# Performance work log

Hardware: AMD Instinct MI355X
Metric: run time of the kernel (lower is better)

The kernel has to match this reference:

```python
import jax, jax.numpy as jnp
import numpy as np

N, D = 8192, 256
TEMP = 0.07


def setup_inputs() -> dict:
    key = jax.random.key(0)
    kx, ky = jax.random.split(key)
    x = jax.random.normal(kx, (N, D), dtype=jnp.float32)
    y = jax.random.normal(ky, (N, D), dtype=jnp.float32)
    # L2-normalize (standard for InfoNCE; keeps exp(sim/temp) finite)
    x = x / jnp.linalg.norm(x, axis=-1, keepdims=True)
    y = y / jnp.linalg.norm(y, axis=-1, keepdims=True)
    return {"x": x, "y": y}


def reference(x, y):
    # sim_matrix = exp(x @ y^T / temperature), shape [N, N]
    sim = jnp.exp(jnp.matmul(x, y.T) / TEMP)
    # positives: exp(<x_i, y_i>/T) == diagonal of sim
    l_pos = jnp.exp(jnp.sum(x * y, axis=-1) / TEMP)
    # negatives: row-sum excluding the diagonal (equivalent to masked_select)
    l_neg = jnp.sum(sim, axis=-1) - jnp.diagonal(sim)
    loss = jnp.mean(-jnp.log(l_pos / l_neg))
    return loss
```

## Files before the change

kernel.cpp:

```cpp
#include <hip/hip_runtime.h>
#include <hip/hip_bf16.h>

#define N_ROWS 8192
#define D_DIM  256

static constexpr float kQuantScale = 64.0f;
static constexpr float kScaleAcc = 20.609929155556627f / 4096.0f;
static constexpr float kInvTAcc  = 14.285714285714286f / 4096.0f;

typedef float f32x4 __attribute__((ext_vector_type(4)));
typedef int   i32x4 __attribute__((ext_vector_type(4)));
typedef int   i32x8 __attribute__((ext_vector_type(8)));

__device__ __forceinline__ void gl_lds16(const void* g, void* l) {
  __builtin_amdgcn_global_load_lds(
      (const __attribute__((address_space(1))) void*)g,
      (__attribute__((address_space(3))) void*)l, 16, 0, 0);
}

__global__ __launch_bounds__(256)
void cvt_fp8_kernel(const float* __restrict__ x, const float* __restrict__ y,
                    unsigned char* __restrict__ xq, unsigned char* __restrict__ yq,
                    float* __restrict__ rowsum, unsigned int* __restrict__ done) {
  if (blockIdx.x == 0) {
    for (int i = threadIdx.x; i < N_ROWS; i += 256) rowsum[i] = 0.f;
    if (threadIdx.x == 0) *done = 0u;
  }
  const int per_mat = N_ROWS * D_DIM / 8;
  int idx = blockIdx.x * blockDim.x + threadIdx.x;
  const float* src = x;
  unsigned char* dst = xq;
  int i = idx;
  if (idx >= per_mat) { src = y; dst = yq; i = idx - per_mat; }
  float4 a = ((const float4*)src)[2 * (size_t)i];
  float4 b = ((const float4*)src)[2 * (size_t)i + 1];
  int v0 = 0, v1 = 0;
  v0 = __builtin_amdgcn_cvt_pk_fp8_f32(a.x * kQuantScale, a.y * kQuantScale, v0, false);
  v0 = __builtin_amdgcn_cvt_pk_fp8_f32(a.z * kQuantScale, a.w * kQuantScale, v0, true);
  v1 = __builtin_amdgcn_cvt_pk_fp8_f32(b.x * kQuantScale, b.y * kQuantScale, v1, false);
  v1 = __builtin_amdgcn_cvt_pk_fp8_f32(b.z * kQuantScale, b.w * kQuantScale, v1, true);
  *(int2*)(dst + (size_t)i * 8) = make_int2(v0, v1);
}

__global__ __launch_bounds__(512, 1)
void infonce_gemm(const unsigned char* __restrict__ X,
                  const unsigned char* __restrict__ Y,
                  float* __restrict__ rowsum, float* __restrict__ diag,
                  unsigned int* __restrict__ done, float* __restrict__ out) {
  __shared__ unsigned char Xs[256 * 256];
  __shared__ unsigned char Ys[2][128 * 256];
  __shared__ unsigned int ticket_s;

  const int b  = blockIdx.x;
  const int bi = b >> 3;
  const int gj = b & 7;

  const int t    = threadIdx.x;
  const int lane = t & 63;
  const int wave = t >> 6;
  const int wm   = wave >> 1;
  const int wn   = wave & 1;
  const int quad = lane >> 4;
  const int l15  = lane & 15;

  const unsigned char* Xblk = X + (size_t)(bi * 256) * D_DIM;

#pragma unroll
  for (int it = 0; it < 8; ++it) {
    const int c0  = (it * 8 + wave) * 64;
    const int s   = c0 + lane;
    const int row = s >> 4;
    const int cg  = (s & 15) ^ (row & 15);
    gl_lds16(Xblk + (size_t)row * D_DIM + cg * 16, &Xs[c0 * 16]);
  }
  {
    const unsigned char* Yblk = Y + (size_t)(gj * 8) * 128 * D_DIM;
#pragma unroll
    for (int it = 0; it < 4; ++it) {
      const int c0  = (it * 8 + wave) * 64;
      const int s   = c0 + lane;
      const int row = s >> 4;
      const int cg  = (s & 15) ^ (row & 15);
      gl_lds16(Yblk + (size_t)row * D_DIM + cg * 16, &Ys[0][c0 * 16]);
    }
  }

  f32x4 acc[4][4];
#pragma unroll
  for (int a = 0; a < 4; ++a)
#pragma unroll
    for (int c = 0; c < 4; ++c) acc[a][c] = (f32x4){0.f, 0.f, 0.f, 0.f};

  float psum[4][4];
#pragma unroll
  for (int a = 0; a < 4; ++a)
#pragma unroll
    for (int c = 0; c < 4; ++c) psum[a][c] = 0.f;

  for (int tt = 0; tt < 8; ++tt) {
    const int p = tt & 1;

    __syncthreads();

    if (tt < 7) {
      const unsigned char* Yblk = Y + (size_t)(gj * 8 + tt + 1) * 128 * D_DIM;
#pragma unroll
      for (int it = 0; it < 4; ++it) {
        const int c0  = (it * 8 + wave) * 64;
        const int s   = c0 + lane;
        const int row = s >> 4;
        const int cg  = (s & 15) ^ (row & 15);
        gl_lds16(Yblk + (size_t)row * D_DIM + cg * 16, &Ys[p ^ 1][c0 * 16]);
      }
    }

#pragma unroll
    for (int kb = 0; kb < 2; ++kb) {
      i32x8 a8[4], b8[4];
#pragma unroll
      for (int mt = 0; mt < 4; ++mt) {
        const int row = wm * 64 + mt * 16 + l15;
        const int p0  = (kb * 8 + quad * 2 + 0) ^ (row & 15);
        const int p1  = (kb * 8 + quad * 2 + 1) ^ (row & 15);
        i32x4 lo = *(const i32x4*)(&Xs[row * 256 + p0 * 16]);
        i32x4 hi = *(const i32x4*)(&Xs[row * 256 + p1 * 16]);
        a8[mt] = __builtin_shufflevector(lo, hi, 0, 1, 2, 3, 4, 5, 6, 7);
      }
#pragma unroll
      for (int nt = 0; nt < 4; ++nt) {
        const int row = wn * 64 + nt * 16 + l15;
        const int p0  = (kb * 8 + quad * 2 + 0) ^ (row & 15);
        const int p1  = (kb * 8 + quad * 2 + 1) ^ (row & 15);
        i32x4 lo = *(const i32x4*)(&Ys[p][row * 256 + p0 * 16]);
        i32x4 hi = *(const i32x4*)(&Ys[p][row * 256 + p1 * 16]);
        b8[nt] = __builtin_shufflevector(lo, hi, 0, 1, 2, 3, 4, 5, 6, 7);
      }
#pragma unroll
      for (int mt = 0; mt < 4; ++mt)
#pragma unroll
        for (int nt = 0; nt < 4; ++nt)
          acc[mt][nt] = __builtin_amdgcn_mfma_scale_f32_16x16x128_f8f6f4(
              a8[mt], b8[nt], acc[mt][nt],
              0, 0,
              0, 0x7F7F7F7F,
              0, 0x7F7F7F7F);
    }

#pragma unroll
    for (int mt = 0; mt < 4; ++mt) {
#pragma unroll
      for (int rr = 0; rr < 4; ++rr) {
        float part = 0.f;
#pragma unroll
        for (int nt = 0; nt < 4; ++nt)
          part += __builtin_amdgcn_exp2f(acc[mt][nt][rr] * kScaleAcc);
        psum[mt][rr] += part;
      }
    }
    {
      const int ct = gj * 8 + tt;
      const bool d0 = (ct == 2 * bi)     && (wm == wn);
      const bool d1 = (ct == 2 * bi + 1) && (wm == wn + 2);
      if (d0 || d1) {
        const int gi_base = bi * 256 + wm * 64;
#pragma unroll
        for (int nt = 0; nt < 4; ++nt)
#pragma unroll
          for (int rr = 0; rr < 4; ++rr)
            if (l15 == quad * 4 + rr)
              atomicExch(&diag[gi_base + nt * 16 + l15], acc[nt][nt][rr]);
      }
    }
#pragma unroll
    for (int a = 0; a < 4; ++a)
#pragma unroll
      for (int c = 0; c < 4; ++c) acc[a][c] = (f32x4){0.f, 0.f, 0.f, 0.f};
  }

  {
    const int gi_base = bi * 256 + wm * 64;
#pragma unroll
    for (int mt = 0; mt < 4; ++mt) {
#pragma unroll
      for (int rr = 0; rr < 4; ++rr) {
        float v = psum[mt][rr];
        v += __shfl_xor(v, 1);
        v += __shfl_xor(v, 2);
        v += __shfl_xor(v, 4);
        v += __shfl_xor(v, 8);
        if (l15 == 0)
          atomicAdd(&rowsum[gi_base + mt * 16 + quad * 4 + rr], v);
      }
    }
  }

  __syncthreads();
  if (t == 0) ticket_s = atomicAdd(done, 1u);
  __syncthreads();
  if (ticket_s == 255u) {
    __threadfence();
    float local = 0.f;
    for (int i = t; i < N_ROWS; i += 512) {
      const float rs = atomicAdd(&rowsum[i], 0.0f);
      const float d  = atomicAdd(&diag[i], 0.0f);
      local += __logf(rs - __builtin_amdgcn_exp2f(d * kScaleAcc)) - d * kInvTAcc;
    }
    float* red = (float*)Xs;
    red[t] = local;
    __syncthreads();
    for (int s2 = 256; s2 > 0; s2 >>= 1) {
      if (t < s2) red[t] += red[t + s2];
      __syncthreads();
    }
    if (t == 0) out[0] = red[0] / (float)N_ROWS;
  }
}

extern "C" void kernel_launch(void* const* d_in, const int* in_sizes, int n_in,
                              void* d_out, int out_size, void* d_ws, size_t ws_size,
                              hipStream_t stream) {
  const float* x = (const float*)d_in[0];
  const float* y = (const float*)d_in[1];
  float* out = (float*)d_out;

  float* rowsum = (float*)d_ws;
  float* diag   = rowsum + N_ROWS;
  unsigned int* done = (unsigned int*)(diag + N_ROWS);
  unsigned char* xq = (unsigned char*)d_ws + 2 * N_ROWS * sizeof(float) + 16;
  unsigned char* yq = xq + (size_t)N_ROWS * D_DIM;

  int cvt_blocks = 2 * N_ROWS * D_DIM / 8 / 256;
  cvt_fp8_kernel<<<cvt_blocks, 256, 0, stream>>>(x, y, xq, yq, rowsum, done);

  infonce_gemm<<<256, 512, 0, stream>>>(xq, yq, rowsum, diag, done, out);
}
```

Before: 101.0 us.

## Add dedicated producer wave for LDS loads with flag-based sync

Adds a ninth wave that performs all global-to-LDS copies of the X and Y tiles, signaling compute waves via LDS ready/consumed counters instead of __syncthreads. Compute waves spin on flags and never issue loads, aiming to overlap loading with MFMA work and remove barrier stalls. The single producer wave serializes loads that previously were spread across eight waves, which may lengthen the prologue; spin-waiting adds scheduling overhead.

```diff
diff --git a/kernel.cpp b/kernel.cpp
--- a/kernel.cpp
+++ b/kernel.cpp
@@ -42,13 +42,15 @@
   *(int2*)(dst + (size_t)i * 8) = make_int2(v0, v1);
 }
 
-__global__ __launch_bounds__(512, 1)
+__global__ __launch_bounds__(576, 1)
 void infonce_gemm(const unsigned char* __restrict__ X,
                   const unsigned char* __restrict__ Y,
                   float* __restrict__ rowsum, float* __restrict__ diag,
                   unsigned int* __restrict__ done, float* __restrict__ out) {
   __shared__ unsigned char Xs[256 * 256];
   __shared__ unsigned char Ys[2][128 * 256];
+  __shared__ int ready[2];
+  __shared__ int consumed[2];
   __shared__ unsigned int ticket_s;
 
   const int b  = blockIdx.x;
@@ -63,133 +65,146 @@
   const int quad = lane >> 4;
   const int l15  = lane & 15;
 
-  const unsigned char* Xblk = X + (size_t)(bi * 256) * D_DIM;
-
-#pragma unroll
-  for (int it = 0; it < 8; ++it) {
-    const int c0  = (it * 8 + wave) * 64;
-    const int s   = c0 + lane;
-    const int row = s >> 4;
-    const int cg  = (s & 15) ^ (row & 15);
-    gl_lds16(Xblk + (size_t)row * D_DIM + cg * 16, &Xs[c0 * 16]);
-  }
-  {
-    const unsigned char* Yblk = Y + (size_t)(gj * 8) * 128 * D_DIM;
-#pragma unroll
-    for (int it = 0; it < 4; ++it) {
-      const int c0  = (it * 8 + wave) * 64;
+  if (t == 0) { ready[0] = -1; ready[1] = -1; consumed[0] = 0; consumed[1] = 0; }
+  __syncthreads();
+
+  if (wave == 8) {
+    const unsigned char* Xblk = X + (size_t)(bi * 256) * D_DIM;
+    for (int it = 0; it < 64; ++it) {
+      const int c0  = it * 64;
       const int s   = c0 + lane;
       const int row = s >> 4;
       const int cg  = (s & 15) ^ (row & 15);
-      gl_lds16(Yblk + (size_t)row * D_DIM + cg * 16, &Ys[0][c0 * 16]);
-    }
-  }
-
-  f32x4 acc[4][4];
-#pragma unroll
-  for (int a = 0; a < 4; ++a)
-#pragma unroll
-    for (int c = 0; c < 4; ++c) acc[a][c] = (f32x4){0.f, 0.f, 0.f, 0.f};
-
-  float psum[4][4];
-#pragma unroll
-  for (int a = 0; a < 4; ++a)
-#pragma unroll
-    for (int c = 0; c < 4; ++c) psum[a][c] = 0.f;
-
-  for (int tt = 0; tt < 8; ++tt) {
-    const int p = tt & 1;
-
-    __syncthreads();
-
-    if (tt < 7) {
-      const unsigned char* Yblk = Y + (size_t)(gj * 8 + tt + 1) * 128 * D_DIM;
-#pragma unroll
-      for (int it = 0; it < 4; ++it) {
-        const int c0  = (it * 8 + wave) * 64;
+      gl_lds16(Xblk + (size_t)row * D_DIM + cg * 16, &Xs[c0 * 16]);
+    }
+    {
+      const unsigned char* Yblk = Y + (size_t)(gj * 8) * 128 * D_DIM;
+      for (int it = 0; it < 32; ++it) {
+        const int c0  = it * 64;
         const int s   = c0 + lane;
         const int row = s >> 4;
         const int cg  = (s & 15) ^ (row & 15);
-        gl_lds16(Yblk + (size_t)row * D_DIM + cg * 16, &Ys[p ^ 1][c0 * 16]);
-      }
-    }
-
-#pragma unroll
-    for (int kb = 0; kb < 2; ++kb) {
-      i32x8 a8[4], b8[4];
+        gl_lds16(Yblk + (size_t)row * D_DIM + cg * 16, &Ys[0][c0 * 16]);
+      }
+    }
+    __builtin_amdgcn_s_waitcnt(0);
+    __hip_atomic_store(&ready[0], 0, __ATOMIC_RELEASE, __HIP_MEMORY_SCOPE_WORKGROUP);
+    for (int r = 1; r < 8; ++r) {
+      const int bb = r & 1;
+      if (r >= 2) {
+        const int need = 8 * (r >> 1);
+        while (__hip_atomic_load(&consumed[bb], __ATOMIC_ACQUIRE,
+                                 __HIP_MEMORY_SCOPE_WORKGROUP) < need)
+          __builtin_amdgcn_s_sleep(2);
+      }
+      const unsigned char* Yblk = Y + (size_t)(gj * 8 + r) * 128 * D_DIM;
+      for (int it = 0; it < 32; ++it) {
+        const int c0  = it * 64;
+        const int s   = c0 + lane;
+        const int row = s >> 4;
+        const int cg  = (s & 15) ^ (row & 15);
+        gl_lds16(Yblk + (size_t)row * D_DIM + cg * 16, &Ys[bb][c0 * 16]);
+      }
+      __builtin_amdgcn_s_waitcnt(0);
+      __hip_atomic_store(&ready[bb], r, __ATOMIC_RELEASE, __HIP_MEMORY_SCOPE_WORKGROUP);
+    }
+  } else {
+    f32x4 acc[4][4];
+#pragma unroll
+    for (int a = 0; a < 4; ++a)
+#pragma unroll
+      for (int c = 0; c < 4; ++c) acc[a][c] = (f32x4){0.f, 0.f, 0.f, 0.f};
+    float psum[4][4];
+#pragma unroll
+    for (int a = 0; a < 4; ++a)
+#pragma unroll
+      for (int c = 0; c < 4; ++c) psum[a][c] = 0.f;
+
+    for (int tt = 0; tt < 8; ++tt) {
+      const int p = tt & 1;
+      while (__hip_atomic_load(&ready[p], __ATOMIC_ACQUIRE,
+                               __HIP_MEMORY_SCOPE_WORKGROUP) < tt)
+        __builtin_amdgcn_s_sleep(1);
+
+#pragma unroll
+      for (int kb = 0; kb < 2; ++kb) {
+        i32x8 a8[4], b8[4];
+#pragma unroll
+        for (int mt = 0; mt < 4; ++mt) {
+          const int row = wm * 64 + mt * 16 + l15;
+          const int p0  = (kb * 8 + quad * 2 + 0) ^ (row & 15);
+          const int p1  = (kb * 8 + quad * 2 + 1) ^ (row & 15);
+          i32x4 lo = *(const i32x4*)(&Xs[row * 256 + p0 * 16]);
+          i32x4 hi = *(const i32x4*)(&Xs[row * 256 + p1 * 16]);
+          a8[mt] = __builtin_shufflevector(lo, hi, 0, 1, 2, 3, 4, 5, 6, 7);
+        }
+#pragma unroll
+        for (int nt = 0; nt < 4; ++nt) {
+          const int row = wn * 64 + nt * 16 + l15;
+          const int p0  = (kb * 8 + quad * 2 + 0) ^ (row & 15);
+          const int p1  = (kb * 8 + quad * 2 + 1) ^ (row & 15);
+          i32x4 lo = *(const i32x4*)(&Ys[p][row * 256 + p0 * 16]);
+          i32x4 hi = *(const i32x4*)(&Ys[p][row * 256 + p1 * 16]);
+          b8[nt] = __builtin_shufflevector(lo, hi, 0, 1, 2, 3, 4, 5, 6, 7);
+        }
+#pragma unroll
+        for (int mt = 0; mt < 4; ++mt)
+#pragma unroll
+          for (int nt = 0; nt < 4; ++nt)
+            acc[mt][nt] = __builtin_amdgcn_mfma_scale_f32_16x16x128_f8f6f4(
+                a8[mt], b8[nt], acc[mt][nt],
+                0, 0, 0, 0x7F7F7F7F, 0, 0x7F7F7F7F);
+      }
+
 #pragma unroll
       for (int mt = 0; mt < 4; ++mt) {
-        const int row = wm * 64 + mt * 16 + l15;
-        const int p0  = (kb * 8 + quad * 2 + 0) ^ (row & 15);
-        const int p1  = (kb * 8 + quad * 2 + 1) ^ (row & 15);
-        i32x4 lo = *(const i32x4*)(&Xs[row * 256 + p0 * 16]);
-        i32x4 hi = *(const i32x4*)(&Xs[row * 256 + p1 * 16]);
-        a8[mt] = __builtin_shufflevector(lo, hi, 0, 1, 2, 3, 4, 5, 6, 7);
-      }
-#pragma unroll
-      for (int nt = 0; nt < 4; ++nt) {
-        const int row = wn * 64 + nt * 16 + l15;
-        const int p0  = (kb * 8 + quad * 2 + 0) ^ (row & 15);
-        const int p1  = (kb * 8 + quad * 2 + 1) ^ (row & 15);
-        i32x4 lo = *(const i32x4*)(&Ys[p][row * 256 + p0 * 16]);
-        i32x4 hi = *(const i32x4*)(&Ys[p][row * 256 + p1 * 16]);
-        b8[nt] = __builtin_shufflevector(lo, hi, 0, 1, 2, 3, 4, 5, 6, 7);
-      }
-#pragma unroll
-      for (int mt = 0; mt < 4; ++mt)
-#pragma unroll
-        for (int nt = 0; nt < 4; ++nt)
-          acc[mt][nt] = __builtin_amdgcn_mfma_scale_f32_16x16x128_f8f6f4(
-              a8[mt], b8[nt], acc[mt][nt],
-              0, 0,
-              0, 0x7F7F7F7F,
-              0, 0x7F7F7F7F);
-    }
-
-#pragma unroll
-    for (int mt = 0; mt < 4; ++mt) {
-#pragma unroll
-      for (int rr = 0; rr < 4; ++rr) {
-        float part = 0.f;
-#pragma unroll
-        for (int nt = 0; nt < 4; ++nt)
-          part += __builtin_amdgcn_exp2f(acc[mt][nt][rr] * kScaleAcc);
-        psum[mt][rr] += part;
-      }
-    }
+#pragma unroll
+        for (int rr = 0; rr < 4; ++rr) {
+          float part = 0.f;
+#pragma unroll
+          for (int nt = 0; nt < 4; ++nt)
+            part += __builtin_amdgcn_exp2f(acc[mt][nt][rr] * kScaleAcc);
+          psum[mt][rr] += part;
+        }
+      }
+      {
+        const int ct = gj * 8 + tt;
+        const bool d0 = (ct == 2 * bi)     && (wm == wn);
+        const bool d1 = (ct == 2 * bi + 1) && (wm == wn + 2);
+        if (d0 || d1) {
+          const int gi_base = bi * 256 + wm * 64;
+#pragma unroll
+          for (int nt = 0; nt < 4; ++nt)
+#pragma unroll
+            for (int rr = 0; rr < 4; ++rr)
+              if (l15 == quad * 4 + rr)
+                atomicExch(&diag[gi_base + nt * 16 + l15], acc[nt][nt][rr]);
+        }
+      }
+#pragma unroll
+      for (int a = 0; a < 4; ++a)
+#pragma unroll
+        for (int c = 0; c < 4; ++c) acc[a][c] = (f32x4){0.f, 0.f, 0.f, 0.f};
+
+      if (lane == 0)
+        __hip_atomic_fetch_add(&consumed[p], 1, __ATOMIC_RELEASE,
+                               __HIP_MEMORY_SCOPE_WORKGROUP);
+    }
+
     {
-      const int ct = gj * 8 + tt;
-      const bool d0 = (ct == 2 * bi)     && (wm == wn);
-      const bool d1 = (ct == 2 * bi + 1) && (wm == wn + 2);
-      if (d0 || d1) {
-        const int gi_base = bi * 256 + wm * 64;
-#pragma unroll
-        for (int nt = 0; nt < 4; ++nt)
-#pragma unroll
-          for (int rr = 0; rr < 4; ++rr)
-            if (l15 == quad * 4 + rr)
-              atomicExch(&diag[gi_base + nt * 16 + l15], acc[nt][nt][rr]);
-      }
-    }
-#pragma unroll
-    for (int a = 0; a < 4; ++a)
-#pragma unroll
-      for (int c = 0; c < 4; ++c) acc[a][c] = (f32x4){0.f, 0.f, 0.f, 0.f};
-  }
-
-  {
-    const int gi_base = bi * 256 + wm * 64;
-#pragma unroll
-    for (int mt = 0; mt < 4; ++mt) {
-#pragma unroll
-      for (int rr = 0; rr < 4; ++rr) {
-        float v = psum[mt][rr];
-        v += __shfl_xor(v, 1);
-        v += __shfl_xor(v, 2);
-        v += __shfl_xor(v, 4);
-        v += __shfl_xor(v, 8);
-        if (l15 == 0)
-          atomicAdd(&rowsum[gi_base + mt * 16 + quad * 4 + rr], v);
+      const int gi_base = bi * 256 + wm * 64;
+#pragma unroll
+      for (int mt = 0; mt < 4; ++mt) {
+#pragma unroll
+        for (int rr = 0; rr < 4; ++rr) {
+          float v = psum[mt][rr];
+          v += __shfl_xor(v, 1);
+          v += __shfl_xor(v, 2);
+          v += __shfl_xor(v, 4);
+          v += __shfl_xor(v, 8);
+          if (l15 == 0)
+            atomicAdd(&rowsum[gi_base + mt * 16 + quad * 4 + rr], v);
+        }
       }
     }
   }
@@ -200,7 +215,7 @@
   if (ticket_s == 255u) {
     __threadfence();
     float local = 0.f;
-    for (int i = t; i < N_ROWS; i += 512) {
+    for (int i = t; i < N_ROWS; i += 576) {
       const float rs = atomicAdd(&rowsum[i], 0.0f);
       const float d  = atomicAdd(&diag[i], 0.0f);
       local += __logf(rs - __builtin_amdgcn_exp2f(d * kScaleAcc)) - d * kInvTAcc;
@@ -208,8 +223,8 @@
     float* red = (float*)Xs;
     red[t] = local;
     __syncthreads();
-    for (int s2 = 256; s2 > 0; s2 >>= 1) {
-      if (t < s2) red[t] += red[t + s2];
+    for (int s2 = 512; s2 > 0; s2 >>= 1) {
+      if (t < s2 && t + s2 < 576) red[t] += red[t + s2];
       __syncthreads();
     }
     if (t == 0) out[0] = red[0] / (float)N_ROWS;
@@ -232,5 +247,5 @@
   int cvt_blocks = 2 * N_ROWS * D_DIM / 8 / 256;
   cvt_fp8_kernel<<<cvt_blocks, 256, 0, stream>>>(x, y, xq, yq, rowsum, done);
 
-  infonce_gemm<<<256, 512, 0, stream>>>(xq, yq, rowsum, diag, done, out);
-}
+  infonce_gemm<<<256, 576, 0, stream>>>(xq, yq, rowsum, diag, done, out);
+}
```

Measured after the change: 116.0 us. 14.9% more time.
